# Optimization experiments

Measured on AMD Instinct MI355X. Metric: run time of the kernel, lower is better.

## Reference

```python
import jax, jax.numpy as jnp
import numpy as np

MINVAL = 0.0
MAXVAL = 1.0


def setup_inputs() -> dict:
    key = jax.random.key(0)
    k1, k2, k3, k4 = jax.random.split(key, 4)
    B, C, G = 16, 16, 4096
    density = jax.random.uniform(k1, (B, 1, G), dtype=jnp.float32)
    xi = jax.random.uniform(k2, (C - 1,), dtype=jnp.float32, minval=-1.0, maxval=1.0)
    grid = jnp.sort(jax.random.uniform(k3, (G,), dtype=jnp.float32))
    grid_weights = jax.random.uniform(k4, (G,), dtype=jnp.float32)
    return {"density": density, "xi": xi, "grid": grid, "grid_weights": grid_weights}


def reference(density, xi, grid, grid_weights):
    # xi -> positive length scales via sigmoid reparameterization
    xi_t = 1.0 / (MINVAL + (MAXVAL - MINVAL) * jax.nn.sigmoid(xi))  # (C-1,)
    # pairwise squared distances on the grid: (G, G)
    g = (grid[:, None] - grid[None, :]) ** 2
    # per-channel Gaussian kernel: (C-1, G, G)
    expo = jnp.exp(-g[None, :, :] * xi_t[:, None, None]) * (0.5 * xi_t[:, None, None])
    # weighted density contracted against each channel kernel: (B, C-1, G)
    integral = jnp.einsum('jkl,ilm->jim', density * grid_weights, expo)
    # append raw density as the last channel: (B, C, G)
    return jnp.concatenate([integral, density], axis=1)
```

## Files before the change

### kernel.cpp

```cpp
#include <hip/hip_runtime.h>
#include <hip/hip_bf16.h>
#include <math.h>


#define RTERMS 32
#define LOG2E 1.4426950408889634f


__global__ void gcl_phaseA(const float* __restrict__ xi, float* __restrict__ ws, int CH) {
    int t = threadIdx.x;
    int Ssz = CH * RTERMS * 16;
    float* aa = ws + Ssz;
    float* sc = aa + CH;
    float* cf = sc + CH;
    for (int j = t; j < Ssz; j += blockDim.x) ws[j] = 0.0f;
    if (t < CH) {
        float xt = 1.0f + __expf(-xi[t]);
        aa[t] = -xt * LOG2E;
        sc[t] = 0.5f * xt;
    }
    if (t < CH * RTERMS) {
        int i = t / RTERMS, n = t % RTERMS;
        float xt = 1.0f + __expf(-xi[i]);
        float z = 2.0f * xt;
        float p = 1.0f, f = 1.0f;
        for (int k = 1; k <= n; ++k) { p *= z; f *= (float)k; }
        cf[t] = p / f;
    }
}

__global__ void gcl_phaseB(const float* __restrict__ density, const float* __restrict__ grid,
                           const float* __restrict__ gw, float* __restrict__ ws,
                           int G, int CH) {
    int i = blockIdx.x;
    int c = blockIdx.y;
    int t = threadIdx.x;
    int b = t >> 4;
    int s = t & 15;
    const float* aa = ws + CH * RTERMS * 16;
    float a = aa[i];

    float acc[RTERMS];
#pragma unroll
    for (int n = 0; n < RTERMS; ++n) acc[n] = 0.0f;

    int chunk = G / gridDim.y;
    int l0 = c * chunk;
    int iters = chunk >> 4;
    for (int it = 0; it < iters; ++it) {
        int l = l0 + it * 16 + s;
        float gl = grid[l];
        float w = density[b * G + l] * gw[l] * exp2f(a * gl * gl);
        float p = w;
#pragma unroll
        for (int n = 0; n < RTERMS; ++n) { acc[n] += p; p *= gl; }
    }

#pragma unroll
    for (int n = 0; n < RTERMS; ++n) {
        float v = acc[n];
        v += __shfl_xor(v, 1, 16);
        v += __shfl_xor(v, 2, 16);
        v += __shfl_xor(v, 4, 16);
        v += __shfl_xor(v, 8, 16);
        acc[n] = v;
    }
    if (s == 0) {
#pragma unroll
        for (int n = 0; n < RTERMS; ++n)
            atomicAdd(&ws[(i * RTERMS + n) * 16 + b], acc[n]);
    }
}

__global__ void gcl_phaseC(const float* __restrict__ density, const float* __restrict__ grid,
                           const float* __restrict__ ws, float* __restrict__ out,
                           int G, int CH) {
    int i = blockIdx.y;
    int b = blockIdx.z;
    int m = blockIdx.x * blockDim.x + threadIdx.x;
    int C = CH + 1;
    if (i == CH) {
        out[(b * C + i) * G + m] = density[b * G + m];
        return;
    }
    const float* aa = ws + CH * RTERMS * 16;
    const float* sc = aa + CH;
    const float* cf = sc + CH;

    __shared__ float T[RTERMS];
    if (threadIdx.x < RTERMS)
        T[threadIdx.x] = cf[i * RTERMS + threadIdx.x] * ws[(i * RTERMS + threadIdx.x) * 16 + b];
    __syncthreads();

    float gm = grid[m];
    float e = exp2f(aa[i] * gm * gm) * sc[i];
    float h = T[RTERMS - 1];
#pragma unroll
    for (int n = RTERMS - 2; n >= 0; --n) h = h * gm + T[n];
    out[(b * C + i) * G + m] = e * h;
}

extern "C" void kernel_launch(void* const* d_in, const int* in_sizes, int n_in,
                              void* d_out, int out_size, void* d_ws, size_t ws_size,
                              hipStream_t stream) {
    const float* density = (const float*)d_in[0];
    const float* xi      = (const float*)d_in[1];
    const float* grid    = (const float*)d_in[2];
    const float* gw      = (const float*)d_in[3];
    float* out = (float*)d_out;
    float* ws  = (float*)d_ws;

    int CH = in_sizes[1];
    int G  = in_sizes[2];
    int B  = in_sizes[0] / G;

    gcl_phaseA<<<1, 512, 0, stream>>>(xi, ws, CH);
    gcl_phaseB<<<dim3(CH, 16), 256, 0, stream>>>(density, grid, gw, ws, G, CH);
    gcl_phaseC<<<dim3(G / 256, CH + 1, B), 256, 0, stream>>>(density, grid, ws, out, G, CH);
}
```

Measured before the change: 75.41 us.

## Drop init kernel, replace atomics with per-chunk partials, shorten Taylor series

Removes the setup kernel. Each kernel now derives its scale factors from xi directly, and the Taylor coefficients come from a fixed inverse-factorial table. The moments kernel writes per-chunk partial sums instead of atomically adding, and the eval kernel sums those partials, which removes the workspace zeroing and the atomic contention. It also doubles the number of grid chunks, cuts the series from 32 to 24 terms, and splits both the power accumulation and the Horner evaluation into independent chains to shorten dependency latency. Truncating the series lowers accuracy for large length-scale factors.

```diff
diff --git a/kernel.cpp b/kernel.cpp
--- a/kernel.cpp
+++ b/kernel.cpp
@@ -3,57 +3,42 @@
 #include <math.h>
 
 
-#define RTERMS 32
+#define RTERMS 24
+#define NC 32
 #define LOG2E 1.4426950408889634f
 
-
-__global__ void gcl_phaseA(const float* __restrict__ xi, float* __restrict__ ws, int CH) {
-    int t = threadIdx.x;
-    int Ssz = CH * RTERMS * 16;
-    float* aa = ws + Ssz;
-    float* sc = aa + CH;
-    float* cf = sc + CH;
-    for (int j = t; j < Ssz; j += blockDim.x) ws[j] = 0.0f;
-    if (t < CH) {
-        float xt = 1.0f + __expf(-xi[t]);
-        aa[t] = -xt * LOG2E;
-        sc[t] = 0.5f * xt;
-    }
-    if (t < CH * RTERMS) {
-        int i = t / RTERMS, n = t % RTERMS;
-        float xt = 1.0f + __expf(-xi[i]);
-        float z = 2.0f * xt;
-        float p = 1.0f, f = 1.0f;
-        for (int k = 1; k <= n; ++k) { p *= z; f *= (float)k; }
-        cf[t] = p / f;
-    }
-}
-
-__global__ void gcl_phaseB(const float* __restrict__ density, const float* __restrict__ grid,
-                           const float* __restrict__ gw, float* __restrict__ ws,
-                           int G, int CH) {
+__global__ void gcl_moments(const float* __restrict__ density, const float* __restrict__ xi,
+                            const float* __restrict__ grid, const float* __restrict__ gw,
+                            float* __restrict__ ws, int G) {
     int i = blockIdx.x;
     int c = blockIdx.y;
     int t = threadIdx.x;
     int b = t >> 4;
     int s = t & 15;
-    const float* aa = ws + CH * RTERMS * 16;
-    float a = aa[i];
+    float xt = 1.0f + __expf(-xi[i]);
+    float a = -xt * LOG2E;
 
     float acc[RTERMS];
 #pragma unroll
     for (int n = 0; n < RTERMS; ++n) acc[n] = 0.0f;
 
-    int chunk = G / gridDim.y;
+    int chunk = G / NC;
     int l0 = c * chunk;
     int iters = chunk >> 4;
     for (int it = 0; it < iters; ++it) {
         int l = l0 + it * 16 + s;
         float gl = grid[l];
         float w = density[b * G + l] * gw[l] * exp2f(a * gl * gl);
-        float p = w;
+        float gl2 = gl * gl;
+        float gl4 = gl2 * gl2;
+        float p0 = w, p1 = w * gl, p2 = w * gl2, p3 = w * gl2 * gl;
 #pragma unroll
-        for (int n = 0; n < RTERMS; ++n) { acc[n] += p; p *= gl; }
+        for (int k = 0; k < RTERMS / 4; ++k) {
+            acc[4 * k + 0] += p0; p0 *= gl4;
+            acc[4 * k + 1] += p1; p1 *= gl4;
+            acc[4 * k + 2] += p2; p2 *= gl4;
+            acc[4 * k + 3] += p3; p3 *= gl4;
+        }
     }
 
 #pragma unroll
@@ -66,38 +51,54 @@
         acc[n] = v;
     }
     if (s == 0) {
+        float* base = ws + ((size_t)(i * NC + c) * RTERMS) * 16 + b;
 #pragma unroll
-        for (int n = 0; n < RTERMS; ++n)
-            atomicAdd(&ws[(i * RTERMS + n) * 16 + b], acc[n]);
+        for (int n = 0; n < RTERMS; ++n) base[n * 16] = acc[n];
     }
 }
 
-__global__ void gcl_phaseC(const float* __restrict__ density, const float* __restrict__ grid,
-                           const float* __restrict__ ws, float* __restrict__ out,
-                           int G, int CH) {
+__global__ void gcl_eval(const float* __restrict__ density, const float* __restrict__ xi,
+                         const float* __restrict__ grid, const float* __restrict__ ws,
+                         float* __restrict__ out, int G, int CH) {
     int i = blockIdx.y;
     int b = blockIdx.z;
     int m = blockIdx.x * blockDim.x + threadIdx.x;
     int C = CH + 1;
     if (i == CH) {
-        out[(b * C + i) * G + m] = density[b * G + m];
+        out[((size_t)b * C + i) * G + m] = density[b * G + m];
         return;
     }
-    const float* aa = ws + CH * RTERMS * 16;
-    const float* sc = aa + CH;
-    const float* cf = sc + CH;
+    float xt = 1.0f + __expf(-xi[i]);
+    float a = -xt * LOG2E;
 
     __shared__ float T[RTERMS];
-    if (threadIdx.x < RTERMS)
-        T[threadIdx.x] = cf[i * RTERMS + threadIdx.x] * ws[(i * RTERMS + threadIdx.x) * 16 + b];
+    if (threadIdx.x < RTERMS) {
+        const float invfact[RTERMS] = {
+            1.0f, 1.0f, 0.5f, 1.6666667e-1f, 4.1666667e-2f, 8.3333333e-3f,
+            1.3888889e-3f, 1.9841270e-4f, 2.4801587e-5f, 2.7557319e-6f,
+            2.7557319e-7f, 2.5052108e-8f, 2.0876757e-9f, 1.6059044e-10f,
+            1.1470746e-11f, 7.6471637e-13f, 4.7794773e-14f, 2.8114573e-15f,
+            1.5619207e-16f, 8.2206352e-18f, 4.1103176e-19f, 1.9572941e-20f,
+            8.8967914e-22f, 3.8681702e-23f};
+        int n = threadIdx.x;
+        float cf = exp2f((float)n * __log2f(2.0f * xt)) * invfact[n];
+        const float* p = ws + ((size_t)(i * NC) * RTERMS + n) * 16 + b;
+        float ssum = 0.0f;
+#pragma unroll
+        for (int cc = 0; cc < NC; ++cc) ssum += p[(size_t)cc * RTERMS * 16];
+        T[n] = cf * ssum;
+    }
     __syncthreads();
 
     float gm = grid[m];
-    float e = exp2f(aa[i] * gm * gm) * sc[i];
-    float h = T[RTERMS - 1];
+    float g2 = gm * gm;
+    float he = T[RTERMS - 2], ho = T[RTERMS - 1];
 #pragma unroll
-    for (int n = RTERMS - 2; n >= 0; --n) h = h * gm + T[n];
-    out[(b * C + i) * G + m] = e * h;
+    for (int k = RTERMS - 4; k >= 0; k -= 2) {
+        he = he * g2 + T[k];
+        ho = ho * g2 + T[k + 1];
+    }
+    out[((size_t)b * C + i) * G + m] = exp2f(a * g2) * (0.5f * xt) * (he + gm * ho);
 }
 
 extern "C" void kernel_launch(void* const* d_in, const int* in_sizes, int n_in,
@@ -114,7 +115,6 @@
     int G  = in_sizes[2];
     int B  = in_sizes[0] / G;
 
-    gcl_phaseA<<<1, 512, 0, stream>>>(xi, ws, CH);
-    gcl_phaseB<<<dim3(CH, 16), 256, 0, stream>>>(density, grid, gw, ws, G, CH);
-    gcl_phaseC<<<dim3(G / 256, CH + 1, B), 256, 0, stream>>>(density, grid, ws, out, G, CH);
+    gcl_moments<<<dim3(CH, NC), 256, 0, stream>>>(density, xi, grid, gw, ws, G);
+    gcl_eval<<<dim3(G / 256, CH + 1, B), 256, 0, stream>>>(density, xi, grid, ws, out, G, CH);
 }
```

New measurement: 73.87 us. -2.0%, faster.
